# Optimization experiments

Measured on AMD Instinct MI355X. Metric: run time of the kernel, lower is better.

## Reference

```python
import jax, jax.numpy as jnp
import numpy as np
from itertools import product

MAX_ALLOC = [3, 3, 3, 3, 3, 3]   # env.maximum_allocation -> 4^6 = 4096 actions
NUM_SESSIONS = 64
STATE_DIM = NUM_SESSIONS + len(MAX_ALLOC)  # 70
HIDDEN = (1024, 1024)
BATCH = 8192


def setup_inputs() -> dict:
    key = jax.random.key(0)
    ks = jax.random.split(key, 8)
    # states: sessions part uniform [0,1); waitlist part uniform [0,4) so mask is nontrivial
    sessions = jax.random.uniform(ks[0], (BATCH, NUM_SESSIONS), dtype=jnp.float32)
    waitlist = jax.random.uniform(ks[1], (BATCH, len(MAX_ALLOC)), dtype=jnp.float32) * 4.0
    states = jnp.concatenate([sessions, waitlist], axis=1)
    # enumerated action space, same order as itertools.product in the torch module
    action_space = jnp.asarray(
        np.array(list(product(*[range(m + 1) for m in MAX_ALLOC])), dtype=np.int32))  # [4096, 6]
    A = action_space.shape[0]
    W1 = jax.random.normal(ks[2], (STATE_DIM, HIDDEN[0]), dtype=jnp.float32) / np.sqrt(STATE_DIM)
    b1 = jnp.zeros((HIDDEN[0],), dtype=jnp.float32)
    W2 = jax.random.normal(ks[3], (HIDDEN[0], HIDDEN[1]), dtype=jnp.float32) / np.sqrt(HIDDEN[0])
    b2 = jnp.zeros((HIDDEN[1],), dtype=jnp.float32)
    Wh = jax.random.normal(ks[4], (HIDDEN[1], A), dtype=jnp.float32) / np.sqrt(HIDDEN[1])
    bh = jnp.zeros((A,), dtype=jnp.float32)
    return {"states": states, "W1": W1, "b1": b1, "W2": W2, "b2": b2,
            "Wh": Wh, "bh": bh, "action_space": action_space,
            "num_sessions": NUM_SESSIONS}


def reference(states, W1, b1, W2, b2, Wh, bh, action_space, num_sessions):
    # vectorized get_action_mask: action j is feasible for row i iff all(action_j <= waitlist_i)
    waitlist = states[:, num_sessions:]                                   # [B, 6]
    feasible = jnp.all(action_space[None, :, :].astype(states.dtype)
                       <= waitlist[:, None, :], axis=-1)                  # [B, A] bool
    mask = feasible.astype(states.dtype)
    # tanh MLP
    h = jnp.tanh(states @ W1 + b1)
    h = jnp.tanh(h @ W2 + b2)
    logits = h @ Wh + bh + jnp.log(mask + 1e-9)                           # [B, A]
    return jax.nn.softmax(logits, axis=1)
```

## Files before the change

kernel.cpp:

```cpp
#include <hip/hip_runtime.h>
#include <hip/hip_bf16.h>
#include <math.h>

using bf16 = __hip_bfloat16;
typedef __attribute__((ext_vector_type(8))) short short8;
typedef __attribute__((ext_vector_type(4))) float f32x4;
typedef __attribute__((ext_vector_type(4))) unsigned int u32x4;

#define BATCH 8192
#define SDIM  70
#define NS    64
#define HID   1024
#define NA    4096
#define KPAD  128

__device__ __forceinline__ void gld_lds16(const bf16* g, bf16* l) {
    __builtin_amdgcn_global_load_lds(
        (const __attribute__((address_space(1))) void*)g,
        (__attribute__((address_space(3))) void*)l, 16, 0, 0);
}

__device__ __forceinline__ void tr32(const float* __restrict__ in, bf16* __restrict__ out,
                                     int K, int N, int Kpad, int bx, int by, int t,
                                     float (*tile)[33]) {
    int kb = by * 32, nb = bx * 32;
    int tx = t & 31, ty = t >> 5;
    #pragma unroll
    for (int i = 0; i < 32; i += 8) {
        int k = kb + ty + i, n = nb + tx;
        tile[ty + i][tx] = (k < K) ? in[(size_t)k * N + n] : 0.0f;
    }
    __syncthreads();
    #pragma unroll
    for (int i = 0; i < 32; i += 8) {
        int n = nb + ty + i, k = kb + tx;
        if (k < Kpad) out[(size_t)n * Kpad + k] = __float2bfloat16(tile[tx][ty + i]);
    }
}

__global__ __launch_bounds__(256)
void prep_k(const float* __restrict__ states, const float* __restrict__ W1,
            const float* __restrict__ W2, const float* __restrict__ Wh,
            const int* __restrict__ act,
            bf16* __restrict__ statesb, bf16* __restrict__ w1bt,
            bf16* __restrict__ w2bt, bf16* __restrict__ whbt,
            unsigned* __restrict__ pact) {
    __shared__ float tile[32][33];
    const int b = blockIdx.x, t = threadIdx.x;
    if (b < 4096) {
        int idx = b * 256 + t;
        int row = idx >> 7, col = idx & 127;
        float v = (col < SDIM) ? states[row * SDIM + col] : 0.0f;
        statesb[idx] = __float2bfloat16(v);
    } else if (b < 4224) {
        int r = b - 4096;
        tr32(W1, w1bt, SDIM, HID, KPAD, r & 31, r >> 5, t, tile);
    } else if (b < 5248) {
        int r = b - 4224;
        tr32(W2, w2bt, HID, HID, HID, r & 31, r >> 5, t, tile);
    } else if (b < 9344) {
        int r = b - 5248;
        tr32(Wh, whbt, HID, NA, HID, r & 127, r >> 7, t, tile);
    } else {
        int c = (b - 9344) * 256 + t;
        if (c < NA) {
            const int* a = act + c * 6;
            unsigned p = 0;
            #pragma unroll
            for (int i = 0; i < 6; i++) p |= ((unsigned)a[i]) << (5 * i);
            pact[c] = p;
        }
    }
}

template<int MODE>
__global__ __launch_bounds__(256)
void gemm128(const bf16* __restrict__ A, const bf16* __restrict__ BT,
             const float* __restrict__ bias, void* __restrict__ Cout,
             int M, int N, int K) {
    const int n0 = blockIdx.x * 128;
    const int m0 = blockIdx.y * 128;
    const int tid  = threadIdx.x;
    const int wave = tid >> 6;
    const int lane = tid & 63;

    __shared__ __align__(16) bf16 As[128 * 64];
    __shared__ __align__(16) bf16 Bs[128 * 64];

    const int lr = lane >> 3;
    const int gk = ((lane & 7) ^ lr) * 8;
    const bf16* ag = A  + (size_t)(m0 + lr) * K + gk;
    const bf16* bg = BT + (size_t)(n0 + lr) * K + gk;

    f32x4 acc[4][4];
    #pragma unroll
    for (int i = 0; i < 4; i++)
        #pragma unroll
        for (int j = 0; j < 4; j++) acc[i][j] = (f32x4){0.f, 0.f, 0.f, 0.f};

    const int rb = (wave >> 1) * 64;
    const int cb = (wave & 1) * 64;
    const int fr = lane & 15;
    const int kq = lane >> 4;

    for (int k0 = 0; k0 < K; k0 += 64) {
        #pragma unroll
        for (int q = 0; q < 4; q++) {
            const int ch = q * 4 + wave;
            gld_lds16(ag + (size_t)(ch * 8) * K + k0, &As[ch * 512]);
            gld_lds16(bg + (size_t)(ch * 8) * K + k0, &Bs[ch * 512]);
        }
        __syncthreads();

        #pragma unroll
        for (int kk = 0; kk < 2; kk++) {
            const int cbase = kk * 4 + kq;
            short8 af[4], bfr[4];
            #pragma unroll
            for (int i = 0; i < 4; i++) {
                int r = rb + i * 16 + fr;
                af[i] = *(const short8*)&As[r * 64 + ((cbase ^ (r & 7)) * 8)];
            }
            #pragma unroll
            for (int j = 0; j < 4; j++) {
                int r = cb + j * 16 + fr;
                bfr[j] = *(const short8*)&Bs[r * 64 + ((cbase ^ (r & 7)) * 8)];
            }
            #pragma unroll
            for (int i = 0; i < 4; i++)
                #pragma unroll
                for (int j = 0; j < 4; j++)
                    acc[i][j] = __builtin_amdgcn_mfma_f32_16x16x32_bf16(af[i], bfr[j], acc[i][j], 0, 0, 0);
        }
        __syncthreads();
    }

    const int orow = m0 + rb + (lane >> 4) * 4;
    const int ocol = n0 + cb + fr;
    #pragma unroll
    for (int j = 0; j < 4; j++) {
        int col = ocol + j * 16;
        float bv = bias[col];
        #pragma unroll
        for (int i = 0; i < 4; i++) {
            int rbase = orow + i * 16;
            #pragma unroll
            for (int r = 0; r < 4; r++) {
                float val = acc[i][j][r] + bv;
                size_t off = (size_t)(rbase + r) * N + col;
                if (MODE == 0)      ((bf16*)Cout)[off] = __float2bfloat16(tanhf(val));
                else if (MODE == 1) ((float*)Cout)[off] = val;
                else                ((bf16*)Cout)[off] = __float2bfloat16(val);
            }
        }
    }
}

__global__ __launch_bounds__(256)
void masked_softmax_k(const bf16* __restrict__ logitsb, float* __restrict__ out,
                      const float* __restrict__ states,
                      const unsigned* __restrict__ pact) {
    const int row  = blockIdx.x;
    const int t    = threadIdx.x;
    const int lane = t & 63, wave = t >> 6;

    __shared__ float redm[4], reds[4];
    __shared__ float smax, ssum;

    const float* wl = states + (size_t)row * SDIM + NS;
    unsigned T = 0;
    #pragma unroll
    for (int i = 0; i < 6; i++) T |= ((unsigned)(int)wl[i]) << (5 * i);
    const unsigned H  = 0x21084210u;
    const unsigned TH = T | H;

    const unsigned* lrow = (const unsigned*)(logitsb + (size_t)row * NA) + t * 8;
    u32x4 raw0 = *(const u32x4*)lrow;
    u32x4 raw1 = *(const u32x4*)(lrow + 4);
    unsigned rw[8];
    #pragma unroll
    for (int i = 0; i < 4; i++) { rw[i] = raw0[i]; rw[4 + i] = raw1[i]; }

    float v[16];
    #pragma unroll
    for (int i = 0; i < 8; i++) {
        v[2 * i]     = __uint_as_float(rw[i] << 16);
        v[2 * i + 1] = __uint_as_float(rw[i] & 0xffff0000u);
    }

    const unsigned* prow = pact + t * 16;
    float lmax = -1e30f;
    #pragma unroll
    for (int q = 0; q < 4; q++) {
        u32x4 p = *(const u32x4*)(prow + q * 4);
        #pragma unroll
        for (int e = 0; e < 4; e++) {
            int j = q * 4 + e;
            bool f = (((TH - p[e]) & H) == H);
            float lg = v[j] + (f ? 0.0f : -20.7232658f);
            v[j] = lg;
            lmax = fmaxf(lmax, lg);
        }
    }
    #pragma unroll
    for (int o = 32; o > 0; o >>= 1) lmax = fmaxf(lmax, __shfl_down(lmax, o, 64));
    if (lane == 0) redm[wave] = lmax;
    __syncthreads();
    if (t == 0) smax = fmaxf(fmaxf(redm[0], redm[1]), fmaxf(redm[2], redm[3]));
    __syncthreads();
    const float bmax = smax;

    float s = 0.f;
    #pragma unroll
    for (int j = 0; j < 16; j++) { float ev = __expf(v[j] - bmax); v[j] = ev; s += ev; }
    #pragma unroll
    for (int o = 32; o > 0; o >>= 1) s += __shfl_down(s, o, 64);
    if (lane == 0) reds[wave] = s;
    __syncthreads();
    if (t == 0) ssum = reds[0] + reds[1] + reds[2] + reds[3];
    __syncthreads();
    const float inv = 1.0f / ssum;

    float* orow = out + (size_t)row * NA + t * 16;
    #pragma unroll
    for (int q = 0; q < 4; q++) {
        f32x4 o4 = { v[q * 4] * inv, v[q * 4 + 1] * inv,
                     v[q * 4 + 2] * inv, v[q * 4 + 3] * inv };
        *(f32x4*)(orow + q * 4) = o4;
    }
}

extern "C" void kernel_launch(void* const* d_in, const int* in_sizes, int n_in,
                              void* d_out, int out_size, void* d_ws, size_t ws_size,
                              hipStream_t stream) {
    const float* states = (const float*)d_in[0];
    const float* W1 = (const float*)d_in[1];
    const float* b1 = (const float*)d_in[2];
    const float* W2 = (const float*)d_in[3];
    const float* b2 = (const float*)d_in[4];
    const float* Wh = (const float*)d_in[5];
    const float* bh = (const float*)d_in[6];
    const int*   act = (const int*)d_in[7];
    float* out = (float*)d_out;

    char* ws = (char*)d_ws;
    bf16* statesb = (bf16*)ws; ws += (size_t)BATCH * KPAD * 2;
    bf16* w1bt    = (bf16*)ws; ws += (size_t)HID * KPAD * 2;
    bf16* w2bt    = (bf16*)ws; ws += (size_t)HID * HID * 2;
    bf16* whbt    = (bf16*)ws; ws += (size_t)NA * HID * 2;
    bf16* h1      = (bf16*)ws; ws += (size_t)BATCH * HID * 2;
    bf16* h2      = (bf16*)ws; ws += (size_t)BATCH * HID * 2;
    bf16* logitsb = (bf16*)ws; ws += (size_t)BATCH * NA * 2;
    unsigned* pact = (unsigned*)ws; ws += (size_t)NA * 4;

    prep_k<<<9360, 256, 0, stream>>>(states, W1, W2, Wh, act,
                                     statesb, w1bt, w2bt, whbt, pact);

    gemm128<0><<<dim3(HID / 128, BATCH / 128), 256, 0, stream>>>(statesb, w1bt, b1, h1, BATCH, HID, KPAD);
    gemm128<0><<<dim3(HID / 128, BATCH / 128), 256, 0, stream>>>(h1, w2bt, b2, h2, BATCH, HID, HID);
    gemm128<2><<<dim3(NA / 128, BATCH / 128), 256, 0, stream>>>(h2, whbt, bh, logitsb, BATCH, NA, HID);

    masked_softmax_k<<<BATCH, 256, 0, stream>>>(logitsb, out, states, pact);
}
```

Before: 341.0 us.

## Add 256x256-tile 8-wave GEMM with XCD swizzle for head projection

Adds a gemm256 kernel that computes 256x256 output tiles with 512 threads. It uses double-buffered direct global-to-LDS loads staged in quarter-tile steps interleaved with MFMA, swizzled LDS layout, wave priority raising around MFMA, and a workgroup remap so neighbouring tiles land on the same XCD. It replaces the 128-tile GEMM only for the largest layer (8192x4096x1024 head). The goal is more operand reuse per load and better overlap of memory with compute. The cost is higher register and LDS use (128KB LDS) and only 512 workgroups.

```diff
diff --git a/kernel.cpp b/kernel.cpp
--- a/kernel.cpp
+++ b/kernel.cpp
@@ -156,6 +156,134 @@
     }
 }
 
+template<int MODE>
+__global__ __launch_bounds__(512)
+void gemm256(const bf16* __restrict__ A, const bf16* __restrict__ BT,
+             const float* __restrict__ bias, void* __restrict__ Cout,
+             int M, int N, int K) {
+    const int nwg = gridDim.x;
+    const int cpx = nwg >> 3;
+    const int wg  = blockIdx.x;
+    const int swz = (wg & 7) * cpx + (wg >> 3);
+    const int gx  = N >> 8;
+    const int n0  = (swz % gx) * 256;
+    const int m0  = (swz / gx) * 256;
+
+    const int tid = threadIdx.x;
+    const int w   = tid >> 6;
+    const int l   = tid & 63;
+    const int wm  = w >> 2;
+    const int wn  = w & 3;
+    const int fr  = l & 15;
+    const int kq  = l >> 4;
+
+    __shared__ __align__(16) bf16 As[2][256 * 64];
+    __shared__ __align__(16) bf16 Bs[2][256 * 64];
+
+    const int lr  = l >> 3;
+    const int ls  = l & 7;
+    const int gkc = (ls ^ lr) * 8;
+
+    const bf16* aAg = A  + (size_t)(m0 + lr) * K + gkc;
+    const bf16* aBg = BT + (size_t)(n0 + lr) * K + gkc;
+
+    f32x4 acc[8][4];
+    #pragma unroll
+    for (int i = 0; i < 8; i++)
+        #pragma unroll
+        for (int j = 0; j < 4; j++) acc[i][j] = (f32x4){0.f, 0.f, 0.f, 0.f};
+
+    const int NT = K >> 6;
+
+    auto STAGE_A = [&](int b, int mh, int k0) {
+        #pragma unroll
+        for (int j = 0; j < 2; j++) {
+            const int rb = j * 128 + mh * 64 + w * 8;
+            gld_lds16(aAg + (size_t)rb * K + k0, &As[b][rb * 64]);
+        }
+    };
+    auto STAGE_B = [&](int b, int nh, int k0) {
+        #pragma unroll
+        for (int j = 0; j < 2; j++) {
+            const int c  = w * 2 + j;
+            const int rb = (c >> 2) * 64 + nh * 32 + (c & 3) * 8;
+            gld_lds16(aBg + (size_t)rb * K + k0, &Bs[b][rb * 64]);
+        }
+    };
+
+    STAGE_A(0, 0, 0); STAGE_B(0, 0, 0); STAGE_A(0, 1, 0); STAGE_B(0, 1, 0);
+    STAGE_B(1, 0, 64); STAGE_A(1, 0, 64);
+    asm volatile("s_waitcnt vmcnt(4)" ::: "memory");
+    __builtin_amdgcn_s_barrier();
+
+    for (int t = 0; t < NT; t++) {
+        const int buf = t & 1;
+        const int kn1 = (t + 1 < NT ? t + 1 : NT - 1) * 64;
+        const int kn2 = (t + 2 < NT ? t + 2 : NT - 1) * 64;
+        #pragma unroll
+        for (int q = 0; q < 4; q++) {
+            const int mh = q & 1;
+            const int nh = q >> 1;
+            short8 af[2][4], bfr[2][2];
+            #pragma unroll
+            for (int kk = 0; kk < 2; kk++) {
+                const int sl = ((kk * 4 + kq) ^ (fr & 7)) * 8;
+                #pragma unroll
+                for (int i = 0; i < 4; i++) {
+                    const int r = wm * 128 + mh * 64 + i * 16 + fr;
+                    af[kk][i] = *(const short8*)&As[buf][r * 64 + sl];
+                }
+                #pragma unroll
+                for (int j = 0; j < 2; j++) {
+                    const int r = wn * 64 + nh * 32 + j * 16 + fr;
+                    bfr[kk][j] = *(const short8*)&Bs[buf][r * 64 + sl];
+                }
+            }
+            if      (q == 0) STAGE_A(buf ^ 1, 1, kn1);
+            else if (q == 1) STAGE_B(buf ^ 1, 1, kn1);
+            else if (q == 2) STAGE_B(buf,     0, kn2);
+            else             STAGE_A(buf,     0, kn2);
+
+            __builtin_amdgcn_s_barrier();
+            asm volatile("s_waitcnt lgkmcnt(0)" ::: "memory");
+            __builtin_amdgcn_s_setprio(1);
+            #pragma unroll
+            for (int kk = 0; kk < 2; kk++)
+                #pragma unroll
+                for (int i = 0; i < 4; i++)
+                    #pragma unroll
+                    for (int j = 0; j < 2; j++)
+                        acc[mh * 4 + i][nh * 2 + j] =
+                            __builtin_amdgcn_mfma_f32_16x16x32_bf16(
+                                af[kk][i], bfr[kk][j],
+                                acc[mh * 4 + i][nh * 2 + j], 0, 0, 0);
+            __builtin_amdgcn_s_setprio(0);
+            if (q == 3) asm volatile("s_waitcnt vmcnt(4)" ::: "memory");
+            __builtin_amdgcn_s_barrier();
+        }
+    }
+
+    const int orow = m0 + wm * 128 + kq * 4;
+    const int ocol = n0 + wn * 64 + fr;
+    #pragma unroll
+    for (int nj = 0; nj < 4; nj++) {
+        const int col = ocol + nj * 16;
+        const float bv = bias[col];
+        #pragma unroll
+        for (int mi = 0; mi < 8; mi++) {
+            const int rbase = orow + mi * 16;
+            #pragma unroll
+            for (int r = 0; r < 4; r++) {
+                const float val = acc[mi][nj][r] + bv;
+                const size_t off = (size_t)(rbase + r) * N + col;
+                if (MODE == 0)      ((bf16*)Cout)[off] = __float2bfloat16(tanhf(val));
+                else if (MODE == 1) ((float*)Cout)[off] = val;
+                else                ((bf16*)Cout)[off] = __float2bfloat16(val);
+            }
+        }
+    }
+}
+
 __global__ __launch_bounds__(256)
 void masked_softmax_k(const bf16* __restrict__ logitsb, float* __restrict__ out,
                       const float* __restrict__ states,
@@ -258,7 +386,8 @@
 
     gemm128<0><<<dim3(HID / 128, BATCH / 128), 256, 0, stream>>>(statesb, w1bt, b1, h1, BATCH, HID, KPAD);
     gemm128<0><<<dim3(HID / 128, BATCH / 128), 256, 0, stream>>>(h1, w2bt, b2, h2, BATCH, HID, HID);
-    gemm128<2><<<dim3(NA / 128, BATCH / 128), 256, 0, stream>>>(h2, whbt, bh, logitsb, BATCH, NA, HID);
+
+    gemm256<2><<<(NA / 256) * (BATCH / 256), 512, 0, stream>>>(h2, whbt, bh, logitsb, BATCH, NA, HID);
 
     masked_softmax_k<<<BATCH, 256, 0, stream>>>(logitsb, out, states, pact);
 }
```

Measured after the change: 371.0 us. +8.8%, slower.
